# Kernel tuning notes

Measured on AMD Instinct MI355X. Metric: run time of the kernel, lower is better.

The kernel has to match this reference:

```python
import jax, jax.numpy as jnp
import numpy as np

DILATIONS = [2 ** i for i in range(9)] * 3  # 27 layers
RD, SD, QD = 32, 512, 256


def conv1d(x, w, b, dilation=1, padding=0):
    # x: [B,C,T], w: [O,I,K], b: [O]
    out = jax.lax.conv_general_dilated(
        x, w, window_strides=(1,), padding=[(padding, padding)],
        rhs_dilation=(dilation,), dimension_numbers=('NCH', 'OIH', 'NCH'))
    return out + b[None, :, None]


def setup_inputs() -> dict:
    key = jax.random.key(0)
    ks = jax.random.split(key, 16)
    T = 131072
    L = len(DILATIONS)
    s = 0.05
    inp = {
        'x': jax.random.normal(ks[0], (1, 1, T), dtype=jnp.float32),
        'Wc': jax.random.normal(ks[1], (RD, 1, 3), dtype=jnp.float32) * s,
        'bc': jnp.zeros((RD,), dtype=jnp.float32),
        'Wt': jax.random.normal(ks[2], (L, RD, RD, 3), dtype=jnp.float32) * s,
        'bt': jnp.zeros((L, RD), dtype=jnp.float32),
        'Ws': jax.random.normal(ks[3], (L, RD, RD, 3), dtype=jnp.float32) * s,
        'bs': jnp.zeros((L, RD), dtype=jnp.float32),
        'Wskip': jax.random.normal(ks[4], (L, SD, RD, 1), dtype=jnp.float32) * s,
        'bskip': jnp.zeros((L, SD), dtype=jnp.float32),
        'Wdense': jax.random.normal(ks[5], (L, RD, RD, 1), dtype=jnp.float32) * s,
        'bdense': jnp.zeros((L, RD), dtype=jnp.float32),
        'Wp1': jax.random.normal(ks[6], (SD, SD, 1), dtype=jnp.float32) * s,
        'bp1': jnp.zeros((SD,), dtype=jnp.float32),
        'Wp2': jax.random.normal(ks[7], (QD, SD, 1), dtype=jnp.float32) * s,
        'bp2': jnp.zeros((QD,), dtype=jnp.float32),
    }
    return inp


def reference(x, Wc, bc, Wt, bt, Ws, bs, Wskip, bskip, Wdense, bdense, Wp1, bp1, Wp2, bp2):
    # causal conv: kernel 3, padding 1 (same length)
    x = conv1d(x, Wc, bc, dilation=1, padding=1)  # [1, RD, T]
    skip = jnp.zeros((1, SD, x.shape[2]), dtype=jnp.float32)
    for i, d in enumerate(DILATIONS):
        xin = x
        g = jnp.tanh(conv1d(x, Wt[i], bt[i], d, d)) * jax.nn.sigmoid(conv1d(x, Ws[i], bs[i], d, d))
        skip = skip + conv1d(g, Wskip[i], bskip[i])
        x = conv1d(g, Wdense[i], bdense[i]) + xin
    # NOTE: the original applies F.relu(x) on the residual path but then
    # overwrites x with the skip-path result, so that relu is dead code.
    out = conv1d(jax.nn.relu(conv1d(skip, Wp1, bp1)), Wp2, bp2)  # [1, QD, T]
    return jax.nn.log_softmax(out, axis=1)
```

## Files before the change

kernel.cpp:

```cpp
#include <hip/hip_runtime.h>

#define T_LEN 131072
#define RD 32
#define SD 512
#define QD 256
#define NL 27
#define KTOT (NL * RD)
#define GPAD 256

typedef __attribute__((ext_vector_type(8))) short short8;
typedef __attribute__((ext_vector_type(4))) float floatx4;

__device__ __forceinline__ unsigned short f2bf(float f) {
    union { float f; unsigned int i; } v; v.f = f;
    unsigned int r = v.i + 0x7fffu + ((v.i >> 16) & 1u);
    return (unsigned short)(r >> 16);
}

__device__ __forceinline__ float bf2f(unsigned short h) {
    union { unsigned int i; float f; } u; u.i = (unsigned int)h << 16;
    return u.f;
}

__device__ __forceinline__ void gload_lds16(const void* g, void* l) {
    __builtin_amdgcn_global_load_lds(
        (const __attribute__((address_space(1))) unsigned int*)g,
        (__attribute__((address_space(3))) unsigned int*)l, 16, 0, 0);
}

__global__ __launch_bounds__(256)
void k_conv_init(const float* __restrict__ x, const float* __restrict__ Wc,
                 const float* __restrict__ bc,
                 unsigned short* __restrict__ xahG, unsigned short* __restrict__ xalG,
                 unsigned short* __restrict__ xbhG)
{
    const int gid = blockIdx.x * 256 + threadIdx.x;

    if (gid < 4 * GPAD * RD) {
        const int region = gid >> 13;
        const int idx = gid & (GPAD * RD - 1);
        unsigned short* hg;
        const size_t post = (size_t)(GPAD + T_LEN) * RD;
        switch (region) {
            case 0:  hg = xahG;        break;
            case 1:  hg = xahG + post; break;
            case 2:  hg = xbhG;        break;
            default: hg = xbhG + post; break;
        }
        hg[idx] = 0;
    }

    const int t = gid;
    const float xm = (t > 0) ? x[t - 1] : 0.f;
    const float x0 = x[t];
    const float xp = (t < T_LEN - 1) ? x[t + 1] : 0.f;
    unsigned short* rowh = xahG + (size_t)(GPAD + t) * RD;
    unsigned short* rowl = xalG + (size_t)(GPAD + t) * RD;
#pragma unroll
    for (int o = 0; o < RD; ++o) {
        const float v = bc[o] + Wc[o * 3 + 0] * xm + Wc[o * 3 + 1] * x0 + Wc[o * 3 + 2] * xp;
        const unsigned short h = f2bf(v);
        rowh[o] = h;
        rowl[o] = f2bf(v - bf2f(h));
    }
}

__global__ __launch_bounds__(256)
void k_wprep(const float* __restrict__ Wt, const float* __restrict__ Ws,
             const float* __restrict__ Wd,
             unsigned short* __restrict__ Wg, unsigned short* __restrict__ Wdb)
{
    const int idx = blockIdx.x * 256 + threadIdx.x;
    const int n1 = NL * 64 * 96;
    const int n2 = NL * RD * RD;
    if (idx < n1) {
        const int l = idx / (64 * 96);
        const int rem = idx % (64 * 96);
        const int m = rem / 96;
        const int k = rem % 96;
        const int j = k / 32;
        const int c = k % 32;
        float v;
        if (m < 32) v = Wt[(((size_t)l * RD + m) * RD + c) * 3 + j];
        else        v = Ws[(((size_t)l * RD + (m - 32)) * RD + c) * 3 + j];
        Wg[idx] = f2bf(v);
    } else if (idx < n1 + n2) {
        const int i2 = idx - n1;
        Wdb[i2] = f2bf(Wd[i2]);
    }
}

__global__ __launch_bounds__(256, 4)
void k_layer_stage(const unsigned short* __restrict__ xinh,
                   const unsigned short* __restrict__ xinl,
                   unsigned short* __restrict__ xouth,
                   unsigned short* __restrict__ xoutl,
                   unsigned short* __restrict__ Gt,
                   const unsigned short* __restrict__ Wg,
                   const unsigned short* __restrict__ Wdb,
                   const float* __restrict__ bt, const float* __restrict__ bs,
                   const float* __restrict__ bd, int d, int layer)
{
    __shared__ unsigned short bandsL[3][128 * 32];
    __shared__ unsigned short loL[128 * 32];
    __shared__ unsigned short gtileL[128 * 32];

    const int tid = threadIdx.x;
    const int lane = tid & 63;
    const int w = tid >> 6;
    const int quad = lane >> 4;
    const int l16 = lane & 15;
    const int rbase = w * 32;
    const bool last = (layer == NL - 1);
    const floatx4 vzero = {0.f, 0.f, 0.f, 0.f};

    const int r16c = lane >> 2;
    const int scB = (lane & 3) ^ ((lane >> 3) & 3);
    const long long gbase = (long long)blockIdx.x * 128 + rbase;

#pragma unroll
    for (int j = 0; j < 3; ++j) {
        const long long b0 = gbase + (long long)(j - 1) * d;
#pragma unroll
        for (int i = 0; i < 2; ++i)
            gload_lds16(xinh + (b0 + i * 16 + r16c) * RD + scB * 8,
                        &bandsL[j][(rbase + i * 16) * 32]);
    }
    asm volatile("" ::: "memory");

    if (!last) {
#pragma unroll
        for (int i = 0; i < 2; ++i)
            gload_lds16(xinl + (gbase + i * 16 + r16c) * RD + scB * 8,
                        &loL[(rbase + i * 16) * 32]);
        asm volatile("s_waitcnt vmcnt(2)" ::: "memory");
    } else {
        asm volatile("s_waitcnt vmcnt(0)" ::: "memory");
    }

    short8 afr[3][4];
#pragma unroll
    for (int j = 0; j < 3; ++j)
#pragma unroll
        for (int mt = 0; mt < 4; ++mt)
            afr[j][mt] = *reinterpret_cast<const short8*>(
                Wg + (size_t)(mt * 16 + l16) * 96 + j * 32 + quad * 8);

    floatx4 acc[4][2];
#pragma unroll
    for (int mt = 0; mt < 4; ++mt)
#pragma unroll
        for (int nt = 0; nt < 2; ++nt) acc[mt][nt] = vzero;

#pragma unroll
    for (int nt = 0; nt < 2; ++nt) {
        const int rloc = rbase + nt * 16 + l16;
        const int key2 = (rloc >> 1) & 3;
#pragma unroll
        for (int j = 0; j < 3; ++j) {
            const short8 bb = *reinterpret_cast<const short8*>(
                &bandsL[j][rloc * 32 + ((quad ^ key2) * 8)]);
#pragma unroll
            for (int mt = 0; mt < 4; ++mt)
                acc[mt][nt] = __builtin_amdgcn_mfma_f32_16x16x32_bf16(
                    afr[j][mt], bb, acc[mt][nt], 0, 0, 0);
        }
    }

    if (!last) asm volatile("s_waitcnt vmcnt(0)" ::: "memory");

#pragma unroll
    for (int nt = 0; nt < 2; ++nt) {
        const int rloc = rbase + nt * 16 + l16;
        const int key2 = (rloc >> 1) & 3;
        const long long t = (long long)blockIdx.x * 128 + rloc;
#pragma unroll
        for (int pair = 0; pair < 2; ++pair) {
            const floatx4 bt4 = *reinterpret_cast<const floatx4*>(bt + pair * 16 + quad * 4);
            const floatx4 bs4 = *reinterpret_cast<const floatx4*>(bs + pair * 16 + quad * 4);
            ushort4 u;
            unsigned short us[4];
#pragma unroll
            for (int r = 0; r < 4; ++r) {
                const float a1 = acc[pair][nt][r] + bt4[r];
                const float a2 = acc[2 + pair][nt][r] + bs4[r];
                const float th = 1.f - __fdividef(2.f, __expf(2.f * a1) + 1.f);
                const float sg = __fdividef(1.f, 1.f + __expf(-a2));
                us[r] = f2bf(th * sg);
            }
            u.x = us[0]; u.y = us[1]; u.z = us[2]; u.w = us[3];
            const int cbase = pair * 16 + quad * 4;
            if (!last) {
                const int colS = (pair * 2 + (quad >> 1)) ^ key2;
                *reinterpret_cast<ushort4*>(
                    &gtileL[rloc * 32 + colS * 8 + (quad & 1) * 4]) = u;
            }
            *reinterpret_cast<ushort4*>(
                Gt + ((size_t)layer * T_LEN + t) * RD + cbase) = u;
        }
    }

    if (!last) {
        short8 ad[2];
#pragma unroll
        for (int mt = 0; mt < 2; ++mt)
            ad[mt] = *reinterpret_cast<const short8*>(
                Wdb + (size_t)(mt * 16 + l16) * RD + quad * 8);

#pragma unroll
        for (int nt = 0; nt < 2; ++nt) {
            const int rloc = rbase + nt * 16 + l16;
            const int key2 = (rloc >> 1) & 3;
            const long long t = (long long)blockIdx.x * 128 + rloc;
            const short8 bg = *reinterpret_cast<const short8*>(
                &gtileL[rloc * 32 + ((quad ^ key2) * 8)]);
#pragma unroll
            for (int mt = 0; mt < 2; ++mt) {
                const floatx4 a2v = __builtin_amdgcn_mfma_f32_16x16x32_bf16(
                    ad[mt], bg, vzero, 0, 0, 0);
                const int m = mt * 16 + quad * 4;
                const int colS2 = (mt * 2 + (quad >> 1)) ^ key2;
                const int off = rloc * 32 + colS2 * 8 + (quad & 1) * 4;
                const ushort4 hi4 = *reinterpret_cast<const ushort4*>(&bandsL[1][off]);
                const ushort4 lo4 = *reinterpret_cast<const ushort4*>(&loL[off]);
                const floatx4 bd4 = *reinterpret_cast<const floatx4*>(bd + m);
                float o0 = a2v[0] + bd4[0] + bf2f(hi4.x) + bf2f(lo4.x);
                float o1 = a2v[1] + bd4[1] + bf2f(hi4.y) + bf2f(lo4.y);
                float o2 = a2v[2] + bd4[2] + bf2f(hi4.z) + bf2f(lo4.z);
                float o3 = a2v[3] + bd4[3] + bf2f(hi4.w) + bf2f(lo4.w);
                ushort4 oh, ol;
                oh.x = f2bf(o0); ol.x = f2bf(o0 - bf2f(oh.x));
                oh.y = f2bf(o1); ol.y = f2bf(o1 - bf2f(oh.y));
                oh.z = f2bf(o2); ol.z = f2bf(o2 - bf2f(oh.z));
                oh.w = f2bf(o3); ol.w = f2bf(o3 - bf2f(oh.w));
                *reinterpret_cast<ushort4*>(xouth + (size_t)t * RD + m) = oh;
                *reinterpret_cast<ushort4*>(xoutl + (size_t)t * RD + m) = ol;
            }
        }
    }
}

__global__ __launch_bounds__(256)
void k_wcomb(const float* __restrict__ Wp1, const float* __restrict__ Wskip,
             unsigned short* __restrict__ Wcomb)
{
    const int idx = blockIdx.x * 256 + threadIdx.x;
    if (idx >= SD * KTOT) return;
    const int m = idx / KTOT;
    const int k = idx % KTOT;
    const int l = k / RD;
    const int c = k % RD;
    const float* wp1r = Wp1 + (size_t)m * SD;
    const float* wsk = Wskip + (size_t)l * SD * RD + c;
    float acc = 0.f;
    for (int j = 0; j < SD; ++j) acc += wp1r[j] * wsk[(size_t)j * RD];
    Wcomb[((size_t)l * SD + m) * RD + c] = f2bf(acc);
}

__global__ __launch_bounds__(512)
void k_hbias(const float* __restrict__ Wp1, const float* __restrict__ bp1,
             const float* __restrict__ bskip, float* __restrict__ hbias)
{
    __shared__ float sb[SD];
    const int tid = threadIdx.x;
    float s = 0.f;
    for (int l = 0; l < NL; ++l) s += bskip[l * SD + tid];
    sb[tid] = s;
    __syncthreads();
    float acc = bp1[tid];
    const float* r = Wp1 + (size_t)tid * SD;
    for (int j = 0; j < SD; ++j) acc += r[j] * sb[j];
    hbias[tid] = acc;
}

__global__ __launch_bounds__(256)
void k_cvt(const float* __restrict__ src, unsigned short* __restrict__ dst, int n)
{
    const int i = blockIdx.x * 256 + threadIdx.x;
    if (i < n) dst[i] = f2bf(src[i]);
}

__global__ __launch_bounds__(256)
void k_gemm1(const unsigned short* __restrict__ A,
             const unsigned short* __restrict__ B,
             const float* __restrict__ hbias,
             unsigned short* __restrict__ ht)
{
    __shared__ unsigned short ldsA[2][128 * 32];
    __shared__ unsigned short ldsB[2][128 * 32];
    const int tid = threadIdx.x;
    const int lane = tid & 63;
    const int w = tid >> 6;
    const int wm = w & 1;
    const int wn = w >> 1;
    const int quad = lane >> 4;
    const int l16 = lane & 15;

    const int g = blockIdx.x;
    const int m0 = ((g >> 3) & 3) * 128;
    const int n0 = ((g & 7) + 8 * (g >> 5)) * 128;

    const int r4 = lane >> 2;
    const int c4 = lane & 3;
    const int srcc = c4 ^ ((r4 >> 1) & 3);
    const int swz = (l16 >> 1) & 3;

    floatx4 acc[4][4];
    const floatx4 vzero = {0.f, 0.f, 0.f, 0.f};
#pragma unroll
    for (int mt = 0; mt < 4; ++mt)
#pragma unroll
        for (int nt = 0; nt < 4; ++nt) acc[mt][nt] = vzero;

    const unsigned short* pA = A + (size_t)(m0 + r4) * RD + srcc * 8;
    const unsigned short* pB = B + (size_t)(n0 + r4) * RD + srcc * 8;

    for (int kc2 = 0; kc2 < 13; ++kc2) {
#pragma unroll
        for (int s = 0; s < 2; ++s) {
            const int kc = kc2 * 2 + s;
#pragma unroll
            for (int c = 0; c < 2; ++c) {
                const int row = w * 32 + c * 16;
                gload_lds16(pA + ((size_t)kc * SD + row) * RD, &ldsA[s][row * 32]);
                gload_lds16(pB + ((size_t)kc * T_LEN + row) * RD, &ldsB[s][row * 32]);
            }
        }
        __syncthreads();

#pragma unroll
        for (int s = 0; s < 2; ++s) {
            short8 afr[4], bfr[4];
#pragma unroll
            for (int mt = 0; mt < 4; ++mt)
                afr[mt] = *reinterpret_cast<const short8*>(
                    &ldsA[s][(wm * 64 + mt * 16 + l16) * 32 + (quad ^ swz) * 8]);
#pragma unroll
            for (int nt = 0; nt < 4; ++nt)
                bfr[nt] = *reinterpret_cast<const short8*>(
                    &ldsB[s][(wn * 64 + nt * 16 + l16) * 32 + (quad ^ swz) * 8]);
#pragma unroll
            for (int mt = 0; mt < 4; ++mt)
#pragma unroll
                for (int nt = 0; nt < 4; ++nt)
                    acc[mt][nt] = __builtin_amdgcn_mfma_f32_16x16x32_bf16(
                        afr[mt], bfr[nt], acc[mt][nt], 0, 0, 0);
        }
        __syncthreads();
    }
    {
        const int kc = 26;
#pragma unroll
        for (int c = 0; c < 2; ++c) {
            const int row = w * 32 + c * 16;
            gload_lds16(pA + ((size_t)kc * SD + row) * RD, &ldsA[0][row * 32]);
            gload_lds16(pB + ((size_t)kc * T_LEN + row) * RD, &ldsB[0][row * 32]);
        }
        __syncthreads();
        short8 afr[4], bfr[4];
#pragma unroll
        for (int mt = 0; mt < 4; ++mt)
            afr[mt] = *reinterpret_cast<const short8*>(
                &ldsA[0][(wm * 64 + mt * 16 + l16) * 32 + (quad ^ swz) * 8]);
#pragma unroll
        for (int nt = 0; nt < 4; ++nt)
            bfr[nt] = *reinterpret_cast<const short8*>(
                &ldsB[0][(wn * 64 + nt * 16 + l16) * 32 + (quad ^ swz) * 8]);
#pragma unroll
        for (int mt = 0; mt < 4; ++mt)
#pragma unroll
            for (int nt = 0; nt < 4; ++nt)
                acc[mt][nt] = __builtin_amdgcn_mfma_f32_16x16x32_bf16(
                    afr[mt], bfr[nt], acc[mt][nt], 0, 0, 0);
    }

#pragma unroll
    for (int mt = 0; mt < 4; ++mt) {
        const int m = m0 + wm * 64 + mt * 16 + quad * 4;
        const floatx4 hb = *reinterpret_cast<const floatx4*>(hbias + m);
        const size_t chunkbase = (size_t)(m >> 5) * T_LEN;
        const int mc = m & 31;
#pragma unroll
        for (int nt = 0; nt < 4; ++nt) {
            const int t = n0 + wn * 64 + nt * 16 + l16;
            ushort4 st;
            float v;
            v = acc[mt][nt][0] + hb[0]; st.x = f2bf(v > 0.f ? v : 0.f);
            v = acc[mt][nt][1] + hb[1]; st.y = f2bf(v > 0.f ? v : 0.f);
            v = acc[mt][nt][2] + hb[2]; st.z = f2bf(v > 0.f ? v : 0.f);
            v = acc[mt][nt][3] + hb[3]; st.w = f2bf(v > 0.f ? v : 0.f);
            *reinterpret_cast<ushort4*>(ht + (chunkbase + t) * RD + mc) = st;
        }
    }
}

__global__ __launch_bounds__(256)
void k_gemm2_lsm(const unsigned short* __restrict__ A,
                 const unsigned short* __restrict__ B,
                 const float* __restrict__ bp2,
                 float* __restrict__ out)
{
    __shared__ unsigned short ldsB[4][64 * 32];
    __shared__ float redmax[4 * 16 * 16];
    __shared__ float redsum[4 * 16 * 16];
    const int tid = threadIdx.x;
    const int lane = tid & 63;
    const int w = tid >> 6;
    const int quad = lane >> 4;
    const int l16 = lane & 15;
    const int m0 = w * 64;
    const int n0 = blockIdx.x * 64;

    const int r4 = lane >> 2;
    const int c4 = lane & 3;
    const int srcc = c4 ^ ((r4 >> 1) & 3);
    const int swz = (l16 >> 1) & 3;

    const unsigned short* ab[4];
#pragma unroll
    for (int mt = 0; mt < 4; ++mt)
        ab[mt] = A + (size_t)(m0 + mt * 16 + l16) * SD + quad * 8;

    const unsigned short* pB = B + (size_t)(n0 + w * 16 + r4) * RD + srcc * 8;

    floatx4 acc[4][4];
    const floatx4 vzero = {0.f, 0.f, 0.f, 0.f};
#pragma unroll
    for (int mt = 0; mt < 4; ++mt)
#pragma unroll
        for (int nt = 0; nt < 4; ++nt) acc[mt][nt] = vzero;

    for (int kc4 = 0; kc4 < 4; ++kc4) {
#pragma unroll
        for (int s = 0; s < 4; ++s)
            gload_lds16(pB + (size_t)(kc4 * 4 + s) * T_LEN * RD,
                        &ldsB[s][(w * 16) * 32]);
        __syncthreads();

#pragma unroll
        for (int s = 0; s < 4; ++s) {
            const int kc = kc4 * 4 + s;
            short8 afr[4];
#pragma unroll
            for (int mt = 0; mt < 4; ++mt)
                afr[mt] = *reinterpret_cast<const short8*>(ab[mt] + kc * 32);
            short8 bfr[4];
#pragma unroll
            for (int nt = 0; nt < 4; ++nt)
                bfr[nt] = *reinterpret_cast<const short8*>(
                    &ldsB[s][(nt * 16 + l16) * 32 + (quad ^ swz) * 8]);
#pragma unroll
            for (int mt = 0; mt < 4; ++mt)
#pragma unroll
                for (int nt = 0; nt < 4; ++nt)
                    acc[mt][nt] = __builtin_amdgcn_mfma_f32_16x16x32_bf16(
                        afr[mt], bfr[nt], acc[mt][nt], 0, 0, 0);
        }
        __syncthreads();
    }

#pragma unroll
    for (int mt = 0; mt < 4; ++mt) {
        const int mb = m0 + mt * 16 + quad * 4;
        const floatx4 bz = *reinterpret_cast<const floatx4*>(bp2 + mb);
#pragma unroll
        for (int nt = 0; nt < 4; ++nt)
#pragma unroll
            for (int j = 0; j < 4; ++j) acc[mt][nt][j] += bz[j];
    }

#pragma unroll
    for (int nt = 0; nt < 4; ++nt) {
        float lm = -1e30f;
#pragma unroll
        for (int mt = 0; mt < 4; ++mt)
#pragma unroll
            for (int j = 0; j < 4; ++j) lm = fmaxf(lm, acc[mt][nt][j]);
        redmax[nt * 256 + l16 * 16 + w * 4 + quad] = lm;
    }
    __syncthreads();

    float lse[4];
#pragma unroll
    for (int nt = 0; nt < 4; ++nt) {
        float gm = -1e30f;
#pragma unroll
        for (int i = 0; i < 16; ++i) gm = fmaxf(gm, redmax[nt * 256 + l16 * 16 + i]);
        float ls = 0.f;
#pragma unroll
        for (int mt = 0; mt < 4; ++mt)
#pragma unroll
            for (int j = 0; j < 4; ++j) ls += __expf(acc[mt][nt][j] - gm);
        redsum[nt * 256 + l16 * 16 + w * 4 + quad] = ls;
        lse[nt] = gm;
    }
    __syncthreads();

#pragma unroll
    for (int nt = 0; nt < 4; ++nt) {
        float tot = 0.f;
#pragma unroll
        for (int i = 0; i < 16; ++i) tot += redsum[nt * 256 + l16 * 16 + i];
        lse[nt] = lse[nt] + __logf(tot);
    }

#pragma unroll
    for (int mt = 0; mt < 4; ++mt) {
        const int mb = m0 + mt * 16 + quad * 4;
#pragma unroll
        for (int nt = 0; nt < 4; ++nt) {
            const int t = n0 + nt * 16 + l16;
#pragma unroll
            for (int j = 0; j < 4; ++j)
                out[(size_t)(mb + j) * T_LEN + t] = acc[mt][nt][j] - lse[nt];
        }
    }
}

extern "C" void kernel_launch(void* const* d_in, const int* in_sizes, int n_in,
                              void* d_out, int out_size, void* d_ws, size_t ws_size,
                              hipStream_t stream)
{
    (void)in_sizes; (void)n_in; (void)out_size; (void)ws_size;
    const float* x     = (const float*)d_in[0];
    const float* Wc    = (const float*)d_in[1];
    const float* bc    = (const float*)d_in[2];
    const float* Wt    = (const float*)d_in[3];
    const float* bt    = (const float*)d_in[4];
    const float* Ws    = (const float*)d_in[5];
    const float* bs    = (const float*)d_in[6];
    const float* Wskip = (const float*)d_in[7];
    const float* bskip = (const float*)d_in[8];
    const float* Wd    = (const float*)d_in[9];
    const float* bd    = (const float*)d_in[10];
    const float* Wp1   = (const float*)d_in[11];
    const float* bp1   = (const float*)d_in[12];
    const float* Wp2   = (const float*)d_in[13];
    const float* bp2   = (const float*)d_in[14];
    float* out = (float*)d_out;

    char* p = (char*)d_ws;
    unsigned short* Gt = (unsigned short*)p;    p += (size_t)T_LEN * KTOT * 2;
    unsigned short* ht = (unsigned short*)p;    p += (size_t)T_LEN * SD * 2;
    unsigned short* Wcomb = (unsigned short*)p; p += (size_t)SD * KTOT * 2;
    unsigned short* Wp2b = (unsigned short*)p;  p += (size_t)QD * SD * 2;
    unsigned short* Wg = (unsigned short*)p;    p += (size_t)NL * 64 * 96 * 2;
    unsigned short* Wdb = (unsigned short*)p;   p += (size_t)NL * RD * RD * 2;
    float* hbias = (float*)p;                   p += (size_t)SD * 4;

    char* q = (char*)ht;
    const size_t grows = (size_t)(T_LEN + 2 * GPAD) * RD;
    unsigned short* xahG = (unsigned short*)q;  q += grows * 2;
    unsigned short* xalG = (unsigned short*)q;  q += grows * 2;
    unsigned short* xbhG = (unsigned short*)q;  q += grows * 2;
    unsigned short* xblG = (unsigned short*)q;  q += grows * 2;
    unsigned short* xah = xahG + (size_t)GPAD * RD;
    unsigned short* xal = xalG + (size_t)GPAD * RD;
    unsigned short* xbh = xbhG + (size_t)GPAD * RD;
    unsigned short* xbl = xblG + (size_t)GPAD * RD;

    k_wcomb<<<(SD * KTOT + 255) / 256, 256, 0, stream>>>(Wp1, Wskip, Wcomb);
    k_hbias<<<1, 512, 0, stream>>>(Wp1, bp1, bskip, hbias);
    k_cvt<<<(QD * SD + 255) / 256, 256, 0, stream>>>(Wp2, Wp2b, QD * SD);
    {
        const int nprep = NL * 64 * 96 + NL * RD * RD;
        k_wprep<<<(nprep + 255) / 256, 256, 0, stream>>>(Wt, Ws, Wd, Wg, Wdb);
    }
    k_conv_init<<<T_LEN / 256, 256, 0, stream>>>(x, Wc, bc, xahG, xalG, xbhG);

    static const int dil[NL] = {1, 2, 4, 8, 16, 32, 64, 128, 256,
                                1, 2, 4, 8, 16, 32, 64, 128, 256,
                                1, 2, 4, 8, 16, 32, 64, 128, 256};
    const unsigned short* curh = xah;
    const unsigned short* curl = xal;
    unsigned short* nxth = xbh;
    unsigned short* nxtl = xbl;
    for (int i = 0; i < NL; ++i) {
        k_layer_stage<<<T_LEN / 128, 256, 0, stream>>>(
            curh, curl, nxth, nxtl, Gt,
            Wg + (size_t)i * 64 * 96,
            Wdb + (size_t)i * RD * RD,
            bt + (size_t)i * RD,
            bs + (size_t)i * RD,
            bd + (size_t)i * RD,
            dil[i], i);
        { unsigned short* th = (unsigned short*)curh; curh = nxth; nxth = th; }
        { unsigned short* tl = (unsigned short*)curl; curl = nxtl; nxtl = tl; }
    }

    k_gemm1<<<4 * (T_LEN / 128), 256, 0, stream>>>(Wcomb, Gt, hbias, ht);
    k_gemm2_lsm<<<T_LEN / 64, 256, 0, stream>>>(Wp2b, ht, bp2, out);
}
```

Measured before the change: 894.9 us.

## Fuse first four dilated layers of each stack into one halo-recomputing kernel

Adds a k_chain4 kernel that runs the dilation 1, 2, 4 and 8 layers back-to-back inside one launch. Each wave loads a 64-row window (32 owned rows plus 16 halo rows per side) and keeps the residual in registers and the bf16 activations in LDS between layers. Only the final layer writes the hi/lo residual split to global memory, and only owned rows write the gate outputs. This removes three launches and three global round-trips of the residual per stack, at the cost of computing twice as many rows for those layers because of the halo. The zero-padding in the init kernel is extended to the low-part buffers because the fused kernel now reads them in the halo region.

```diff
diff --git a/kernel.cpp b/kernel.cpp
--- a/kernel.cpp
+++ b/kernel.cpp
@@ -32,11 +32,11 @@
 void k_conv_init(const float* __restrict__ x, const float* __restrict__ Wc,
                  const float* __restrict__ bc,
                  unsigned short* __restrict__ xahG, unsigned short* __restrict__ xalG,
-                 unsigned short* __restrict__ xbhG)
+                 unsigned short* __restrict__ xbhG, unsigned short* __restrict__ xblG)
 {
     const int gid = blockIdx.x * 256 + threadIdx.x;
 
-    if (gid < 4 * GPAD * RD) {
+    if (gid < 8 * GPAD * RD) {
         const int region = gid >> 13;
         const int idx = gid & (GPAD * RD - 1);
         unsigned short* hg;
@@ -45,7 +45,11 @@
             case 0:  hg = xahG;        break;
             case 1:  hg = xahG + post; break;
             case 2:  hg = xbhG;        break;
-            default: hg = xbhG + post; break;
+            case 3:  hg = xbhG + post; break;
+            case 4:  hg = xalG;        break;
+            case 5:  hg = xalG + post; break;
+            case 6:  hg = xblG;        break;
+            default: hg = xblG + post; break;
         }
         hg[idx] = 0;
     }
@@ -91,6 +95,166 @@
 }
 
 __global__ __launch_bounds__(256, 4)
+void k_chain4(const unsigned short* __restrict__ xinh,
+              const unsigned short* __restrict__ xinl,
+              unsigned short* __restrict__ xouth,
+              unsigned short* __restrict__ xoutl,
+              unsigned short* __restrict__ Gt,
+              const unsigned short* __restrict__ WgAll,
+              const unsigned short* __restrict__ WdbAll,
+              const float* __restrict__ btAll,
+              const float* __restrict__ bsAll,
+              const float* __restrict__ bdAll,
+              int l0)
+{
+    __shared__ unsigned short segA[4][64 * 32];
+    __shared__ unsigned short segB[4][64 * 32];
+    __shared__ unsigned short gsc[4][16 * 32];
+    const int tid = threadIdx.x;
+    const int lane = tid & 63;
+    const int w = tid >> 6;
+    const int quad = lane >> 4;
+    const int l16 = lane & 15;
+    const long long t0 = (long long)blockIdx.x * 128 + w * 32;
+    const long long Wb = t0 - 16;
+    const floatx4 vzero = {0.f, 0.f, 0.f, 0.f};
+    const int key2g = (l16 >> 1) & 3;
+
+    const int r16c = lane >> 2;
+    const int scB = (lane & 3) ^ ((lane >> 3) & 3);
+#pragma unroll
+    for (int i = 0; i < 4; ++i)
+        gload_lds16(xinh + (Wb + i * 16 + r16c) * RD + scB * 8,
+                    &segA[w][(i * 16) * 32]);
+    asm volatile("" ::: "memory");
+
+    floatx4 x[4][2];
+#pragma unroll
+    for (int s = 0; s < 4; ++s) {
+        const long long t = Wb + s * 16 + l16;
+#pragma unroll
+        for (int mt = 0; mt < 2; ++mt) {
+            const ushort4 h4 = *reinterpret_cast<const ushort4*>(
+                xinh + t * RD + mt * 16 + quad * 4);
+            const ushort4 l4 = *reinterpret_cast<const ushort4*>(
+                xinl + t * RD + mt * 16 + quad * 4);
+            x[s][mt][0] = bf2f(h4.x) + bf2f(l4.x);
+            x[s][mt][1] = bf2f(h4.y) + bf2f(l4.y);
+            x[s][mt][2] = bf2f(h4.z) + bf2f(l4.z);
+            x[s][mt][3] = bf2f(h4.w) + bf2f(l4.w);
+        }
+    }
+    asm volatile("s_waitcnt vmcnt(0)" ::: "memory");
+
+    static const int dd[4] = {1, 2, 4, 8};
+#pragma unroll
+    for (int k = 0; k < 4; ++k) {
+        const int d = dd[k];
+        const int l = l0 + k;
+        const unsigned short* Wg = WgAll + (size_t)l * 64 * 96;
+        const unsigned short* Wdb = WdbAll + (size_t)l * RD * RD;
+        const float* btp = btAll + (size_t)l * RD;
+        const float* bsp = bsAll + (size_t)l * RD;
+        const float* bdp = bdAll + (size_t)l * RD;
+        unsigned short* cur = (k & 1) ? segB[w] : segA[w];
+        unsigned short* nxt = (k & 1) ? segA[w] : segB[w];
+
+        short8 afr[3][4];
+#pragma unroll
+        for (int j = 0; j < 3; ++j)
+#pragma unroll
+            for (int mt = 0; mt < 4; ++mt)
+                afr[j][mt] = *reinterpret_cast<const short8*>(
+                    Wg + (size_t)(mt * 16 + l16) * 96 + j * 32 + quad * 8);
+        short8 ad[2];
+#pragma unroll
+        for (int mt = 0; mt < 2; ++mt)
+            ad[mt] = *reinterpret_cast<const short8*>(
+                Wdb + (size_t)(mt * 16 + l16) * RD + quad * 8);
+
+#pragma unroll
+        for (int s = 0; s < 4; ++s) {
+            floatx4 acc[4];
+#pragma unroll
+            for (int mt = 0; mt < 4; ++mt) acc[mt] = vzero;
+#pragma unroll
+            for (int j = 0; j < 3; ++j) {
+                int lr = s * 16 + l16 + (j - 1) * d;
+                lr = lr < 0 ? 0 : (lr > 63 ? 63 : lr);
+                const short8 bb = *reinterpret_cast<const short8*>(
+                    &cur[lr * 32 + ((quad ^ ((lr >> 1) & 3)) * 8)]);
+#pragma unroll
+                for (int mt = 0; mt < 4; ++mt)
+                    acc[mt] = __builtin_amdgcn_mfma_f32_16x16x32_bf16(
+                        afr[j][mt], bb, acc[mt], 0, 0, 0);
+            }
+
+            const bool owned = (s == 1 || s == 2);
+            const long long tg = t0 + (long long)(s - 1) * 16 + l16;
+#pragma unroll
+            for (int pair = 0; pair < 2; ++pair) {
+                const floatx4 bt4 = *reinterpret_cast<const floatx4*>(btp + pair * 16 + quad * 4);
+                const floatx4 bs4 = *reinterpret_cast<const floatx4*>(bsp + pair * 16 + quad * 4);
+                ushort4 u;
+                unsigned short us[4];
+#pragma unroll
+                for (int r = 0; r < 4; ++r) {
+                    const float a1 = acc[pair][r] + bt4[r];
+                    const float a2 = acc[2 + pair][r] + bs4[r];
+                    const float th = 1.f - __fdividef(2.f, __expf(2.f * a1) + 1.f);
+                    const float sg = __fdividef(1.f, 1.f + __expf(-a2));
+                    us[r] = f2bf(th * sg);
+                }
+                u.x = us[0]; u.y = us[1]; u.z = us[2]; u.w = us[3];
+                const int colS = (pair * 2 + (quad >> 1)) ^ key2g;
+                *reinterpret_cast<ushort4*>(
+                    &gsc[w][l16 * 32 + colS * 8 + (quad & 1) * 4]) = u;
+                if (owned)
+                    *reinterpret_cast<ushort4*>(
+                        Gt + ((size_t)l * T_LEN + tg) * RD + pair * 16 + quad * 4) = u;
+            }
+            asm volatile("s_waitcnt lgkmcnt(0)" ::: "memory");
+            __builtin_amdgcn_sched_barrier(0);
+
+            const short8 bg = *reinterpret_cast<const short8*>(
+                &gsc[w][l16 * 32 + (quad ^ key2g) * 8]);
+            const int lrw = s * 16 + l16;
+            const int key2w = (lrw >> 1) & 3;
+#pragma unroll
+            for (int mt = 0; mt < 2; ++mt) {
+                const floatx4 a2v = __builtin_amdgcn_mfma_f32_16x16x32_bf16(
+                    ad[mt], bg, vzero, 0, 0, 0);
+                const floatx4 bd4 = *reinterpret_cast<const floatx4*>(bdp + mt * 16 + quad * 4);
+                floatx4 xn;
+                xn[0] = a2v[0] + bd4[0] + x[s][mt][0];
+                xn[1] = a2v[1] + bd4[1] + x[s][mt][1];
+                xn[2] = a2v[2] + bd4[2] + x[s][mt][2];
+                xn[3] = a2v[3] + bd4[3] + x[s][mt][3];
+                x[s][mt] = xn;
+                ushort4 oh;
+                oh.x = f2bf(xn[0]); oh.y = f2bf(xn[1]);
+                oh.z = f2bf(xn[2]); oh.w = f2bf(xn[3]);
+                if (k < 3) {
+                    const int colS2 = (mt * 2 + (quad >> 1)) ^ key2w;
+                    *reinterpret_cast<ushort4*>(
+                        &nxt[lrw * 32 + colS2 * 8 + (quad & 1) * 4]) = oh;
+                } else if (owned) {
+                    ushort4 ol;
+                    ol.x = f2bf(xn[0] - bf2f(oh.x));
+                    ol.y = f2bf(xn[1] - bf2f(oh.y));
+                    ol.z = f2bf(xn[2] - bf2f(oh.z));
+                    ol.w = f2bf(xn[3] - bf2f(oh.w));
+                    *reinterpret_cast<ushort4*>(xouth + tg * RD + mt * 16 + quad * 4) = oh;
+                    *reinterpret_cast<ushort4*>(xoutl + tg * RD + mt * 16 + quad * 4) = ol;
+                }
+            }
+            asm volatile("s_waitcnt lgkmcnt(0)" ::: "memory");
+            __builtin_amdgcn_sched_barrier(0);
+        }
+    }
+}
+
+__global__ __launch_bounds__(256, 4)
 void k_layer_stage(const unsigned short* __restrict__ xinh,
                    const unsigned short* __restrict__ xinl,
                    unsigned short* __restrict__ xouth,
@@ -127,7 +291,6 @@
                         &bandsL[j][(rbase + i * 16) * 32]);
     }
     asm volatile("" ::: "memory");
-
     if (!last) {
 #pragma unroll
         for (int i = 0; i < 2; ++i)
@@ -566,26 +729,31 @@
         const int nprep = NL * 64 * 96 + NL * RD * RD;
         k_wprep<<<(nprep + 255) / 256, 256, 0, stream>>>(Wt, Ws, Wd, Wg, Wdb);
     }
-    k_conv_init<<<T_LEN / 256, 256, 0, stream>>>(x, Wc, bc, xahG, xalG, xbhG);
-
-    static const int dil[NL] = {1, 2, 4, 8, 16, 32, 64, 128, 256,
-                                1, 2, 4, 8, 16, 32, 64, 128, 256,
-                                1, 2, 4, 8, 16, 32, 64, 128, 256};
+    k_conv_init<<<T_LEN / 256, 256, 0, stream>>>(x, Wc, bc, xahG, xalG, xbhG, xblG);
+
     const unsigned short* curh = xah;
     const unsigned short* curl = xal;
     unsigned short* nxth = xbh;
     unsigned short* nxtl = xbl;
-    for (int i = 0; i < NL; ++i) {
-        k_layer_stage<<<T_LEN / 128, 256, 0, stream>>>(
-            curh, curl, nxth, nxtl, Gt,
-            Wg + (size_t)i * 64 * 96,
-            Wdb + (size_t)i * RD * RD,
-            bt + (size_t)i * RD,
-            bs + (size_t)i * RD,
-            bd + (size_t)i * RD,
-            dil[i], i);
+    static const int dsing[5] = {16, 32, 64, 128, 256};
+    for (int s = 0; s < 3; ++s) {
+        k_chain4<<<T_LEN / 128, 256, 0, stream>>>(
+            curh, curl, nxth, nxtl, Gt, Wg, Wdb, bt, bs, bd, 9 * s);
         { unsigned short* th = (unsigned short*)curh; curh = nxth; nxth = th; }
         { unsigned short* tl = (unsigned short*)curl; curl = nxtl; nxtl = tl; }
+        for (int j = 0; j < 5; ++j) {
+            const int li = 9 * s + 4 + j;
+            k_layer_stage<<<T_LEN / 128, 256, 0, stream>>>(
+                curh, curl, nxth, nxtl, Gt,
+                Wg + (size_t)li * 64 * 96,
+                Wdb + (size_t)li * RD * RD,
+                bt + (size_t)li * RD,
+                bs + (size_t)li * RD,
+                bd + (size_t)li * RD,
+                dsing[j], li);
+            { unsigned short* th = (unsigned short*)curh; curh = nxth; nxth = th; }
+            { unsigned short* tl = (unsigned short*)curl; curl = nxtl; nxtl = tl; }
+        }
     }
 
     k_gemm1<<<4 * (T_LEN / 128), 256, 0, stream>>>(Wcomb, Gt, hbias, ht);
```

Result: slower. 1.053 ms (+17.7%).
